# Performance work log

Measured on AMD Instinct MI355X. Metric: run time of the kernel, lower is better.

## Reference

```python
import jax, jax.numpy as jnp
import numpy as np

M = 4        # num_modalities
C = 128      # in_channels
NH = 4       # num_heads
HD = C // NH # head_dim = 32
OUT = 128    # out_channels
B, D, H, W = 1, 12, 12, 12
N = D * H * W
EPS = 1e-5
SCALE = float(np.sqrt(HD))


def setup_inputs() -> dict:
    key = jax.random.key(0)
    ks = jax.random.split(key, 12)
    inp = {}
    for i in range(M):
        inp[f"feat{i}"] = jax.random.normal(ks[i], (B, C, D, H, W), dtype=jnp.float32)
    s = 1.0 / np.sqrt(C)
    inp["Wq"] = jax.random.normal(ks[4], (M, C, C), dtype=jnp.float32) * s
    inp["Wk"] = jax.random.normal(ks[5], (M, C, C), dtype=jnp.float32) * s
    inp["Wv"] = jax.random.normal(ks[6], (M, C, C), dtype=jnp.float32) * s
    inp["Wout"] = jax.random.normal(ks[7], (OUT, C), dtype=jnp.float32) * s
    inp["bn_gamma"] = jnp.ones((OUT,), jnp.float32)
    inp["bn_beta"] = jnp.zeros((OUT,), jnp.float32)
    inp["bn_mean"] = jax.random.normal(ks[8], (OUT,), dtype=jnp.float32) * 0.1
    inp["bn_var"] = jax.random.uniform(ks[9], (OUT,), dtype=jnp.float32, minval=0.5, maxval=1.5)
    return inp


def _proj(Wm, feats):
    # per-modality 1x1 conv == matmul over channels: [M,C,C] x [M,B,C,N] -> [M,B,nh,N,hd]
    p = jnp.einsum('moc,mbcn->mbon', Wm, feats)
    return p.reshape(M, B, NH, HD, N).transpose(0, 1, 2, 4, 3)


def reference(feat0, feat1, feat2, feat3, Wq, Wk, Wv, Wout,
              bn_gamma, bn_beta, bn_mean, bn_var):
    feats = jnp.stack([feat0, feat1, feat2, feat3]).reshape(M, B, C, N)
    Q = _proj(Wq, feats)   # [M,B,nh,N,hd]
    K = _proj(Wk, feats)
    V = _proj(Wv, feats)
    # concat K/V over modalities along token axis -> [B,nh,M*N,hd]
    Kall = K.transpose(1, 2, 0, 3, 4).reshape(B, NH, M * N, HD)
    Vall = V.transpose(1, 2, 0, 3, 4).reshape(B, NH, M * N, HD)
    fused = jnp.zeros((B, NH, N, HD), jnp.float32)
    for i in range(M):  # small fixed loop over modalities
        attn = jnp.einsum('bhqd,bhkd->bhqk', Q[i], Kall) / SCALE  # [B,nh,N,M*N]
        attn = jax.nn.softmax(attn, axis=-1)  # dropout is identity at eval
        fused = fused + jnp.einsum('bhqk,bhkd->bhqd', attn, Vall)
    fused = fused.transpose(0, 1, 3, 2).reshape(B, C, N)
    # out_proj: 1x1 Conv3d -> BN (eval, running stats) -> ReLU
    y = jnp.einsum('oc,bcn->bon', Wout, fused)
    inv = bn_gamma / jnp.sqrt(bn_var + EPS)
    y = y * inv[None, :, None] + (bn_beta - bn_mean * inv)[None, :, None]
    return jax.nn.relu(y).reshape(B, OUT, D, H, W)
```

## Files before the change

kernel.cpp:

```cpp
#include <hip/hip_runtime.h>

#define MODS 4
#define CH   128
#define NHD  4
#define HDIM 32
#define NTOK 1728
#define NG   (NTOK/4)
#define NKEY (MODS*NTOK)
#define NT   27
#define QSC (0.17677669529663687f * 1.4426950408889634f)

#ifndef __has_builtin
#define __has_builtin(x) 0
#endif
#if __has_builtin(__builtin_amdgcn_exp2f)
#define EXP2(x) __builtin_amdgcn_exp2f(x)
#else
#define EXP2(x) __expf(0.69314718055994531f * (x))
#endif

typedef __bf16 bf16x8 __attribute__((ext_vector_type(8)));
typedef float  f32x16 __attribute__((ext_vector_type(16)));
typedef unsigned int u32x4 __attribute__((ext_vector_type(4)));

__device__ inline bf16x8 ldb8(const unsigned short* p) {
    return *reinterpret_cast<const bf16x8*>(p);
}
__device__ inline unsigned int pkbf(float a, float b) {
    unsigned short ua = __builtin_bit_cast(unsigned short, (__bf16)a);
    unsigned short ub = __builtin_bit_cast(unsigned short, (__bf16)b);
    return (unsigned int)ua | ((unsigned int)ub << 16);
}
__device__ inline void glds16(const unsigned short* g, unsigned short* l) {
    __builtin_amdgcn_global_load_lds(
        (const __attribute__((address_space(1))) unsigned int*)(g),
        (__attribute__((address_space(3))) unsigned int*)(l), 16, 0, 0);
}

__global__ __launch_bounds__(256) void proj_kernel(
    const float* __restrict__ f0, const float* __restrict__ f1,
    const float* __restrict__ f2, const float* __restrict__ f3,
    const float* __restrict__ Wq, const float* __restrict__ Wk,
    const float* __restrict__ Wv,
    unsigned short* __restrict__ Qb, unsigned short* __restrict__ Kb,
    unsigned short* __restrict__ V2)
{
    __shared__ __align__(16) float Wt[64][68];
    __shared__ __align__(16) float fs[64][68];

    const int tid = threadIdx.x;
    const int bid = blockIdx.x;
    const int tm  = bid / 54;
    const int rem = bid % 54;
    const int oh  = rem & 1;
    const int nt  = rem >> 1;
    const int t   = tm >> 2, m = tm & 3;
    const int nb  = nt * 64;

    const float* fsrc = (m == 0) ? f0 : (m == 1) ? f1 : (m == 2) ? f2 : f3;
    const float* W    = ((t == 0) ? Wq : (t == 1) ? Wk : Wv) + (size_t)m * CH * CH;

    const int o0 = (tid >> 4) * 4, nn0 = (tid & 15) * 4;
    float acc[4][4] = {};

    for (int ch = 0; ch < 2; ++ch) {
        if (ch) __syncthreads();
        {
            const int o = tid & 63, c4b = tid >> 6;
            #pragma unroll
            for (int j = 0; j < 4; ++j) {
                const int c4 = c4b + 4 * j;
                float4 wv = *reinterpret_cast<const float4*>(
                    W + (size_t)(oh * 64 + o) * CH + ch * 64 + c4 * 4);
                Wt[c4*4+0][o] = wv.x; Wt[c4*4+1][o] = wv.y;
                Wt[c4*4+2][o] = wv.z; Wt[c4*4+3][o] = wv.w;
            }
        }
        {
            const int nchunk = tid & 15, cb = tid >> 4;
            #pragma unroll
            for (int j = 0; j < 4; ++j) {
                const int c = cb + 16 * j;
                float4 v = *reinterpret_cast<const float4*>(
                    fsrc + (size_t)(ch * 64 + c) * NTOK + nb + nchunk * 4);
                *reinterpret_cast<float4*>(&fs[c][nchunk * 4]) = v;
            }
        }
        __syncthreads();
        #pragma unroll 4
        for (int c = 0; c < 64; ++c) {
            float4 wv = *reinterpret_cast<const float4*>(&Wt[c][o0]);
            float4 fv = *reinterpret_cast<const float4*>(&fs[c][nn0]);
            acc[0][0] = fmaf(wv.x, fv.x, acc[0][0]); acc[0][1] = fmaf(wv.x, fv.y, acc[0][1]);
            acc[0][2] = fmaf(wv.x, fv.z, acc[0][2]); acc[0][3] = fmaf(wv.x, fv.w, acc[0][3]);
            acc[1][0] = fmaf(wv.y, fv.x, acc[1][0]); acc[1][1] = fmaf(wv.y, fv.y, acc[1][1]);
            acc[1][2] = fmaf(wv.y, fv.z, acc[1][2]); acc[1][3] = fmaf(wv.y, fv.w, acc[1][3]);
            acc[2][0] = fmaf(wv.z, fv.x, acc[2][0]); acc[2][1] = fmaf(wv.z, fv.y, acc[2][1]);
            acc[2][2] = fmaf(wv.z, fv.z, acc[2][2]); acc[2][3] = fmaf(wv.z, fv.w, acc[2][3]);
            acc[3][0] = fmaf(wv.w, fv.x, acc[3][0]); acc[3][1] = fmaf(wv.w, fv.y, acc[3][1]);
            acc[3][2] = fmaf(wv.w, fv.z, acc[3][2]); acc[3][3] = fmaf(wv.w, fv.w, acc[3][3]);
        }
    }

    const int og0 = oh * 64 + o0;
    const int h = og0 >> 5, d0 = og0 & 31;
    const int ng = nb + nn0;
    if (t == 2) {
        const int off = ng & 15;
        const int ng2 = (ng & ~15) + ((off & 4) << 1) + ((off & 8) >> 1);
        #pragma unroll
        for (int i = 0; i < 4; ++i) {
            ushort4 pk;
            pk.x = __builtin_bit_cast(unsigned short, (__bf16)acc[i][0]);
            pk.y = __builtin_bit_cast(unsigned short, (__bf16)acc[i][1]);
            pk.z = __builtin_bit_cast(unsigned short, (__bf16)acc[i][2]);
            pk.w = __builtin_bit_cast(unsigned short, (__bf16)acc[i][3]);
            *reinterpret_cast<ushort4*>(V2 + (size_t)(h * HDIM + d0 + i) * NKEY + m * NTOK + ng2) = pk;
        }
    } else {
        const float sc = (t == 0) ? QSC : 1.0f;
        unsigned short* base = ((t == 0) ? Qb : Kb)
            + (((size_t)(m * NHD + h)) * NTOK + ng) * HDIM + d0;
        #pragma unroll
        for (int j = 0; j < 4; ++j) {
            unsigned short* row = base + (size_t)j * HDIM;
            *reinterpret_cast<unsigned int*>(row)     = pkbf(acc[0][j] * sc, acc[1][j] * sc);
            *reinterpret_cast<unsigned int*>(row + 2) = pkbf(acc[2][j] * sc, acc[3][j] * sc);
        }
    }
}

__global__ __launch_bounds__(512) void attn_kernel(
    const unsigned short* __restrict__ Qb, const unsigned short* __restrict__ Kb,
    const unsigned short* __restrict__ V2,
    float* __restrict__ accT, float* __restrict__ sR)
{
    __shared__ __align__(16) unsigned short smAll[2][2][2][2048];
    __shared__ __align__(16) float sL[4][2][2][32];

    const int tid  = threadIdx.x;
    const int lane = tid & 63;
    const int w    = tid >> 6;
    const int qslot = w & 3;
    const int ks    = w >> 2;
    const int l31  = lane & 31;
    const int hi   = lane >> 5;

    const int bid  = blockIdx.x;
    const int slot = bid & 7;
    const int h    = slot >> 1;
    const int ko   = slot & 1;
    const int qb   = bid >> 3;
    const int qtile = qb * 4 + qslot;
    const int qg0  = qtile * 32;
    const int im   = qg0 / NTOK;
    const int n0   = qg0 % NTOK;
    const int km   = ko * 2 + ks;

    const unsigned short* qp = Qb + (((size_t)(im * NHD + h)) * NTOK + n0 + l31) * HDIM + hi * 8;
    const bf16x8 qf0 = ldb8(qp);
    const bf16x8 qf1 = ldb8(qp + 16);

    unsigned short* sm = &smAll[ks][0][0][0];

    const int rK = qslot * 16 + (lane >> 2);
    const int cK = (lane & 3) ^ ((lane >> 3) & 3);
    const unsigned short* gK = Kb + (((size_t)(km * NHD + h)) * NTOK + rK) * HDIM + cK * 8;
    const int dV = qslot * 8 + (lane >> 3);
    const int cV = (lane & 7) ^ ((lane >> 3) & 7);
    const unsigned short* gV = V2 + ((size_t)(h * HDIM + dV)) * NKEY + km * NTOK + cV * 8;

    const int f31 = (l31 >> 1) & 3;
    const int kA0 = l31 * 32 + ((hi ^ f31) << 3);
    const int kB0 = l31 * 32 + (((2 + hi) ^ f31) << 3);
    const int vbase = l31 * 64;
    const int x7 = l31 & 7;

    f32x16 o_acc;
    #pragma unroll
    for (int r = 0; r < 16; ++r) o_acc[r] = 0.f;
    float s_part = 0.f;
    int buf = 0;

    glds16(gK, sm + qslot * 512);
    glds16(gV, sm + 2048 + qslot * 512);
    __syncthreads();

    for (int t = 0; t < NT; ++t) {
        if (t + 1 < NT) {
            unsigned short* dst = sm + (buf ^ 1) * 4096;
            glds16(gK + (t + 1) * 2048, dst + qslot * 512);
            glds16(gV + (t + 1) * 64,  dst + 2048 + qslot * 512);
        }
        const unsigned short* Kl = sm + buf * 4096;
        const unsigned short* Vl = Kl + 2048;

        #pragma unroll
        for (int st = 0; st < 2; ++st) {
            bf16x8 k0 = ldb8(Kl + st * 1024 + kA0);
            bf16x8 k1 = ldb8(Kl + st * 1024 + kB0);
            f32x16 c;
            #pragma unroll
            for (int r = 0; r < 16; ++r) c[r] = 0.f;
            c = __builtin_amdgcn_mfma_f32_32x32x16_bf16(k0, qf0, c, 0, 0, 0);
            c = __builtin_amdgcn_mfma_f32_32x32x16_bf16(k1, qf1, c, 0, 0, 0);

            float e[16];
            #pragma unroll
            for (int r = 0; r < 16; ++r) { e[r] = EXP2(c[r]); s_part += e[r]; }
            bf16x8 pa0, pa1;
            #pragma unroll
            for (int j = 0; j < 8; ++j) { pa0[j] = (__bf16)e[j]; pa1[j] = (__bf16)e[8 + j]; }

            bf16x8 v0 = ldb8(Vl + vbase + (((4 * st + hi)     ^ x7) << 3));
            bf16x8 v1 = ldb8(Vl + vbase + (((4 * st + 2 + hi) ^ x7) << 3));

            o_acc = __builtin_amdgcn_mfma_f32_32x32x16_bf16(pa0, v0, o_acc, 0, 0, 0);
            o_acc = __builtin_amdgcn_mfma_f32_32x32x16_bf16(pa1, v1, o_acc, 0, 0, 0);
        }
        __syncthreads();
        buf ^= 1;
    }

    float* accf = (float*)&smAll[0][0][0][0];
    if (ks == 1) {
        #pragma unroll
        for (int r = 0; r < 16; ++r) {
            const int qrow = (r & 3) + 8 * (r >> 2) + 4 * hi;
            accf[(qslot * 32 + qrow) * 33 + l31] = o_acc[r];
        }
    }
    sL[qslot][ks][hi][l31] = s_part;
    __syncthreads();
    if (ks == 0) {
        #pragma unroll
        for (int r = 0; r < 16; ++r) {
            const int qrow = (r & 3) + 8 * (r >> 2) + 4 * hi;
            accf[(qslot * 32 + qrow) * 33 + l31] += o_acc[r];
        }
    }
    __syncthreads();
    {
        const int q  = tid & 127;
        const int d0 = tid >> 7;
        #pragma unroll
        for (int j = 0; j < 8; ++j) {
            const int d = d0 + j * 4;
            accT[((size_t)((ko * 4 + h) * HDIM + d)) * NKEY + (size_t)qb * 128 + q]
                = accf[q * 33 + d];
        }
        if (tid < 128) {
            const int qs = tid >> 5, ql = tid & 31;
            float st = (sL[qs][0][0][ql] + sL[qs][0][1][ql])
                     + (sL[qs][1][0][ql] + sL[qs][1][1][ql]);
            sR[((size_t)(ko * 4 + h)) * NKEY + (size_t)qb * 128 + tid] = st;
        }
    }
}

__global__ __launch_bounds__(256) void norm_kernel(
    const float* __restrict__ accT, const float* __restrict__ sR,
    float* __restrict__ fused)
{
    const int idx = blockIdx.x * 256 + threadIdx.x;
    const int c = idx / NTOK;
    const int n = idx % NTOK;
    const int h = c >> 5;
    float acc = 0.f;
    #pragma unroll
    for (int imq = 0; imq < MODS; ++imq) {
        const size_t q = (size_t)imq * NTOK + n;
        const float s = sR[(size_t)h * NKEY + q] + sR[(size_t)(4 + h) * NKEY + q];
        const float a = accT[(size_t)c * NKEY + q] + accT[(size_t)(c + 128) * NKEY + q];
        acc = fmaf(a, 1.0f / s, acc);
    }
    fused[idx] = acc;
}

__global__ __launch_bounds__(256) void outproj_kernel(
    const float* __restrict__ fused, const float* __restrict__ Wout,
    const float* __restrict__ gamma, const float* __restrict__ beta,
    const float* __restrict__ mean,  const float* __restrict__ var,
    float* __restrict__ out)
{
    const int idx = blockIdx.x * 256 + threadIdx.x;
    const int n2 = idx % (NTOK / 2);
    const int o  = idx / (NTOK / 2);
    const float* W     = Wout + (size_t)o * CH;
    const float* fbase = fused + n2 * 2;
    float a0 = 0.f, a1 = 0.f;
    #pragma unroll 8
    for (int c = 0; c < CH; c += 4) {
        float4 w4 = *reinterpret_cast<const float4*>(W + c);
        float2 r0 = *reinterpret_cast<const float2*>(fbase + (size_t)(c + 0) * NTOK);
        float2 r1 = *reinterpret_cast<const float2*>(fbase + (size_t)(c + 1) * NTOK);
        float2 r2 = *reinterpret_cast<const float2*>(fbase + (size_t)(c + 2) * NTOK);
        float2 r3 = *reinterpret_cast<const float2*>(fbase + (size_t)(c + 3) * NTOK);
        a0 = fmaf(w4.x, r0.x, a0); a0 = fmaf(w4.y, r1.x, a0);
        a0 = fmaf(w4.z, r2.x, a0); a0 = fmaf(w4.w, r3.x, a0);
        a1 = fmaf(w4.x, r0.y, a1); a1 = fmaf(w4.y, r1.y, a1);
        a1 = fmaf(w4.z, r2.y, a1); a1 = fmaf(w4.w, r3.y, a1);
    }
    float inv = gamma[o] * rsqrtf(var[o] + 1e-5f);
    float sh  = fmaf(-mean[o], inv, beta[o]);
    float2 y;
    y.x = fmaxf(fmaf(a0, inv, sh), 0.f);
    y.y = fmaxf(fmaf(a1, inv, sh), 0.f);
    *reinterpret_cast<float2*>(out + (size_t)o * NTOK + n2 * 2) = y;
}

extern "C" void kernel_launch(void* const* d_in, const int* in_sizes, int n_in,
                              void* d_out, int out_size, void* d_ws, size_t ws_size,
                              hipStream_t stream)
{
    const float* f0    = (const float*)d_in[0];
    const float* f1    = (const float*)d_in[1];
    const float* f2    = (const float*)d_in[2];
    const float* f3    = (const float*)d_in[3];
    const float* Wq    = (const float*)d_in[4];
    const float* Wk    = (const float*)d_in[5];
    const float* Wv    = (const float*)d_in[6];
    const float* Wout  = (const float*)d_in[7];
    const float* gamma = (const float*)d_in[8];
    const float* beta  = (const float*)d_in[9];
    const float* mean  = (const float*)d_in[10];
    const float* var   = (const float*)d_in[11];
    float* out = (float*)d_out;

    const size_t QKV = (size_t)MODS * NHD * NTOK * HDIM;
    unsigned short* Qb = (unsigned short*)d_ws;
    unsigned short* Kb = Qb + QKV;
    unsigned short* V2 = Kb + QKV;
    float* accT  = (float*)(V2 + QKV);
    float* sR    = accT + (size_t)2 * NHD * HDIM * NKEY;
    float* fused = sR + (size_t)2 * NHD * NKEY;

    proj_kernel<<<648, 256, 0, stream>>>(f0, f1, f2, f3, Wq, Wk, Wv, Qb, Kb, V2);
    attn_kernel<<<432, 512, 0, stream>>>(Qb, Kb, V2, accT, sR);
    norm_kernel<<<(CH * NTOK) / 256, 256, 0, stream>>>(accT, sR, fused);
    outproj_kernel<<<(CH * NTOK / 2) / 256, 256, 0, stream>>>(
        fused, Wout, gamma, beta, mean, var, out);
}
```

Before: 75.92 us.

## Halve attention block size and replace syncthreads with manual waitcnt pipelining

Attention blocks shrink from 512 to 256 threads (2 query tiles instead of 4) and the grid doubles, so each wave now stages twice as much K/V per tile. The single prefetch buffer loop is replaced by loads issued two tiles ahead, with explicit vmcnt/lgkmcnt waits and raw s_barrier so global-to-LDS copies overlap compute more deeply. The aim is to hide memory latency and raise occupancy. In exchange, K/V tiles are loaded twice as often across blocks, and the hand-tuned wait counts must exactly match the number of outstanding loads.

```diff
diff --git a/kernel.cpp b/kernel.cpp
--- a/kernel.cpp
+++ b/kernel.cpp
@@ -130,19 +130,19 @@
     }
 }
 
-__global__ __launch_bounds__(512) void attn_kernel(
+__global__ __launch_bounds__(256) void attn_kernel(
     const unsigned short* __restrict__ Qb, const unsigned short* __restrict__ Kb,
     const unsigned short* __restrict__ V2,
     float* __restrict__ accT, float* __restrict__ sR)
 {
     __shared__ __align__(16) unsigned short smAll[2][2][2][2048];
-    __shared__ __align__(16) float sL[4][2][2][32];
+    __shared__ __align__(16) float sL[2][2][2][32];
 
     const int tid  = threadIdx.x;
     const int lane = tid & 63;
     const int w    = tid >> 6;
-    const int qslot = w & 3;
-    const int ks    = w >> 2;
+    const int qslot = w & 1;
+    const int ks    = w >> 1;
     const int l31  = lane & 31;
     const int hi   = lane >> 5;
 
@@ -151,7 +151,7 @@
     const int h    = slot >> 1;
     const int ko   = slot & 1;
     const int qb   = bid >> 3;
-    const int qtile = qb * 4 + qslot;
+    const int qtile = qb * 2 + qslot;
     const int qg0  = qtile * 32;
     const int im   = qg0 / NTOK;
     const int n0   = qg0 % NTOK;
@@ -161,14 +161,18 @@
     const bf16x8 qf0 = ldb8(qp);
     const bf16x8 qf1 = ldb8(qp + 16);
 
-    unsigned short* sm = &smAll[ks][0][0][0];
-
-    const int rK = qslot * 16 + (lane >> 2);
-    const int cK = (lane & 3) ^ ((lane >> 3) & 3);
-    const unsigned short* gK = Kb + (((size_t)(km * NHD + h)) * NTOK + rK) * HDIM + cK * 8;
-    const int dV = qslot * 8 + (lane >> 3);
-    const int cV = (lane & 7) ^ ((lane >> 3) & 7);
-    const unsigned short* gV = V2 + ((size_t)(h * HDIM + dV)) * NKEY + km * NTOK + cV * 8;
+    const int rk0 = qslot * 32 + (lane >> 2);
+    const int ck0 = (lane & 3) ^ ((rk0 >> 1) & 3);
+    const unsigned short* gK0 = Kb + (((size_t)(km * NHD + h)) * NTOK + rk0) * HDIM + ck0 * 8;
+    const int rk1 = rk0 + 16;
+    const int ck1 = (lane & 3) ^ ((rk1 >> 1) & 3);
+    const unsigned short* gK1 = Kb + (((size_t)(km * NHD + h)) * NTOK + rk1) * HDIM + ck1 * 8;
+    const int dv0 = qslot * 16 + (lane >> 3);
+    const int cv0 = (lane & 7) ^ (dv0 & 7);
+    const unsigned short* gV0 = V2 + ((size_t)(h * HDIM + dv0)) * NKEY + km * NTOK + cv0 * 8;
+    const int dv1 = dv0 + 8;
+    const int cv1 = (lane & 7) ^ (dv1 & 7);
+    const unsigned short* gV1 = V2 + ((size_t)(h * HDIM + dv1)) * NKEY + km * NTOK + cv1 * 8;
 
     const int f31 = (l31 >> 1) & 3;
     const int kA0 = l31 * 32 + ((hi ^ f31) << 3);
@@ -180,20 +184,28 @@
     #pragma unroll
     for (int r = 0; r < 16; ++r) o_acc[r] = 0.f;
     float s_part = 0.f;
-    int buf = 0;
-
-    glds16(gK, sm + qslot * 512);
-    glds16(gV, sm + 2048 + qslot * 512);
-    __syncthreads();
+
+    #define STAGE(tt, bb) do {                                              \
+        unsigned short* _k = &smAll[bb][ks][0][0];                          \
+        glds16(gK0 + (size_t)(tt) * 2048, _k + (qslot * 32) * 32);          \
+        glds16(gK1 + (size_t)(tt) * 2048, _k + (qslot * 32 + 16) * 32);     \
+        unsigned short* _v = &smAll[bb][ks][1][0];                          \
+        glds16(gV0 + (size_t)(tt) * 64,  _v + (qslot * 16) * 64);           \
+        glds16(gV1 + (size_t)(tt) * 64,  _v + (qslot * 16 + 8) * 64);       \
+    } while (0)
+
+    STAGE(0, 0);
+    STAGE(1, 1);
 
     for (int t = 0; t < NT; ++t) {
-        if (t + 1 < NT) {
-            unsigned short* dst = sm + (buf ^ 1) * 4096;
-            glds16(gK + (t + 1) * 2048, dst + qslot * 512);
-            glds16(gV + (t + 1) * 64,  dst + 2048 + qslot * 512);
-        }
-        const unsigned short* Kl = sm + buf * 4096;
-        const unsigned short* Vl = Kl + 2048;
+        if (t < NT - 1) asm volatile("s_waitcnt vmcnt(4)" ::: "memory");
+        else            asm volatile("s_waitcnt vmcnt(0)" ::: "memory");
+        __builtin_amdgcn_sched_barrier(0);
+        __builtin_amdgcn_s_barrier();
+        __builtin_amdgcn_sched_barrier(0);
+
+        const unsigned short* Kl = &smAll[t & 1][ks][0][0];
+        const unsigned short* Vl = &smAll[t & 1][ks][1][0];
 
         #pragma unroll
         for (int st = 0; st < 2; ++st) {
@@ -218,10 +230,16 @@
             o_acc = __builtin_amdgcn_mfma_f32_32x32x16_bf16(pa0, v0, o_acc, 0, 0, 0);
             o_acc = __builtin_amdgcn_mfma_f32_32x32x16_bf16(pa1, v1, o_acc, 0, 0, 0);
         }
-        __syncthreads();
-        buf ^= 1;
-    }
-
+
+        asm volatile("s_waitcnt lgkmcnt(0)" ::: "memory");
+        __builtin_amdgcn_sched_barrier(0);
+        __builtin_amdgcn_s_barrier();
+        __builtin_amdgcn_sched_barrier(0);
+        if (t + 2 < NT) STAGE(t + 2, t & 1);
+    }
+    #undef STAGE
+
+    __syncthreads();
     float* accf = (float*)&smAll[0][0][0][0];
     if (ks == 1) {
         #pragma unroll
@@ -241,19 +259,19 @@
     }
     __syncthreads();
     {
-        const int q  = tid & 127;
-        const int d0 = tid >> 7;
+        const int q  = tid & 63;
+        const int dq = tid >> 6;
         #pragma unroll
         for (int j = 0; j < 8; ++j) {
-            const int d = d0 + j * 4;
-            accT[((size_t)((ko * 4 + h) * HDIM + d)) * NKEY + (size_t)qb * 128 + q]
+            const int d = dq * 8 + j;
+            accT[((size_t)((ko * 4 + h) * HDIM + d)) * NKEY + (size_t)qb * 64 + q]
                 = accf[q * 33 + d];
         }
-        if (tid < 128) {
+        if (tid < 64) {
             const int qs = tid >> 5, ql = tid & 31;
             float st = (sL[qs][0][0][ql] + sL[qs][0][1][ql])
                      + (sL[qs][1][0][ql] + sL[qs][1][1][ql]);
-            sR[((size_t)(ko * 4 + h)) * NKEY + (size_t)qb * 128 + tid] = st;
+            sR[((size_t)(ko * 4 + h)) * NKEY + (size_t)qb * 64 + tid] = st;
         }
     }
 }
@@ -336,7 +354,7 @@
     float* fused = sR + (size_t)2 * NHD * NKEY;
 
     proj_kernel<<<648, 256, 0, stream>>>(f0, f1, f2, f3, Wq, Wk, Wv, Qb, Kb, V2);
-    attn_kernel<<<432, 512, 0, stream>>>(Qb, Kb, V2, accT, sR);
+    attn_kernel<<<864, 256, 0, stream>>>(Qb, Kb, V2, accT, sR);
     norm_kernel<<<(CH * NTOK) / 256, 256, 0, stream>>>(accT, sR, fused);
     outproj_kernel<<<(CH * NTOK / 2) / 256, 256, 0, stream>>>(
         fused, Wout, gamma, beta, mean, var, out);
```

Result: slower. 84.98 us (+11.9%).
